# Optimization experiments

Hardware: AMD Instinct MI355X
Metric: run time of the kernel (lower is better)

Reference implementation:

```python
import jax, jax.numpy as jnp
import numpy as np

ALPHA = 0.2      # LeakyReLU negative slope
EPS = 1e-5       # LayerNorm eps (torch default)
NEG = -9e15      # mask value from the original module

N, IN_F, OUT_F = 8192, 256, 64


def setup_inputs() -> dict:
    key = jax.random.key(0)
    k1, k2, k3, k4, k5 = jax.random.split(key, 5)
    inp = {
        "input": jax.random.normal(k1, (N, IN_F), dtype=jnp.float32),
        "adj": jax.random.randint(k2, (N, N), 0, 2, dtype=jnp.int32),
        "W": jax.random.normal(k3, (IN_F, OUT_F), dtype=jnp.float32) * (1.414 * (6.0 / (IN_F + OUT_F)) ** 0.5),
        "a1": jax.random.normal(k4, (OUT_F,), dtype=jnp.float32) * 0.2,
        "a2": jax.random.normal(k5, (OUT_F,), dtype=jnp.float32) * 0.2,
        "gamma": jnp.ones((OUT_F,), dtype=jnp.float32),
        "beta": jnp.zeros((OUT_F,), dtype=jnp.float32),
    }
    return inp


def reference(input, adj, W, a1, a2, gamma, beta):
    h = input @ W                                    # [N, F]
    # a^T [Wh_i || Wh_j] = (Wh_i @ a1) + (Wh_j @ a2)  (exact decomposition)
    f = h @ a1                                       # [N]
    g = h @ a2                                       # [N]
    e = jax.nn.leaky_relu(f[:, None] + g[None, :], ALPHA)   # [N, N]
    e = jnp.where(adj > 0, e, jnp.float32(NEG))
    attention = jax.nn.softmax(e, axis=1)            # [N, N]  (dropout p=0 -> identity)
    h_prime = attention @ h                          # [N, F]
    # LayerNorm over feature dim
    mu = jnp.mean(h_prime, axis=-1, keepdims=True)
    var = jnp.mean((h_prime - mu) ** 2, axis=-1, keepdims=True)
    h_norm = (h_prime - mu) * jax.lax.rsqrt(var + EPS) * gamma + beta
    return jax.nn.elu(h_norm)                        # concat=True -> ELU
```

## Files before the change

kernel.cpp:

```cpp
#include <hip/hip_runtime.h>
#include <math.h>

#define N      8192
#define IN_F   256
#define OUT_F  64
#define ALPHA  0.2f
#define LN_EPS 1e-5f
#define KVB    256
#define NCH    (N / KVB)

typedef __attribute__((ext_vector_type(8))) short bf16x8;
typedef __attribute__((ext_vector_type(4))) short s16x4;
typedef __attribute__((ext_vector_type(4))) float f32x4;
typedef __attribute__((ext_vector_type(4))) int   i32x4;

__device__ __forceinline__ float wave_sum(float v) {
#pragma unroll
    for (int off = 32; off >= 1; off >>= 1) v += __shfl_xor(v, off, 64);
    return v;
}

__device__ __forceinline__ short f2bf(float x) {
    union { float f; unsigned u; } v; v.f = x;
    unsigned r = v.u + 0x7FFF + ((v.u >> 16) & 1);
    return (short)(r >> 16);
}
__device__ __forceinline__ float bf2f(short b) {
    union { unsigned u; float f; } v; v.u = ((unsigned)(unsigned short)b) << 16;
    return v.f;
}

__global__ __launch_bounds__(256) void gat_phaseA(
    const float* __restrict__ input, const float* __restrict__ W,
    const float* __restrict__ a1, const float* __restrict__ a2,
    unsigned short* __restrict__ hB, float* __restrict__ fv, float* __restrict__ gv)
{
    const int lane = threadIdx.x & 63;
    const int wid  = threadIdx.x >> 6;
    const int blockRow0 = blockIdx.x * 32;
    const int i0 = blockRow0 + wid * 8;

    float hacc[8];
#pragma unroll
    for (int r = 0; r < 8; r++) hacc[r] = 0.f;

    for (int k = 0; k < IN_F; k += 4) {
        const float w0 = W[(k + 0) * OUT_F + lane];
        const float w1 = W[(k + 1) * OUT_F + lane];
        const float w2 = W[(k + 2) * OUT_F + lane];
        const float w3 = W[(k + 3) * OUT_F + lane];
#pragma unroll
        for (int r = 0; r < 8; r++) {
            const float4 iv = *(const float4*)&input[(size_t)(i0 + r) * IN_F + k];
            hacc[r] = fmaf(iv.x, w0, hacc[r]);
            hacc[r] = fmaf(iv.y, w1, hacc[r]);
            hacc[r] = fmaf(iv.z, w2, hacc[r]);
            hacc[r] = fmaf(iv.w, w3, hacc[r]);
        }
    }

    const float a1v = a1[lane];
    const float a2v = a2[lane];

    __shared__ float hsm[32][65];
#pragma unroll
    for (int r = 0; r < 8; r++) {
        hsm[wid * 8 + r][lane] = hacc[r];
        const float fr = wave_sum(hacc[r] * a1v);
        const float gr = wave_sum(hacc[r] * a2v);
        if (lane == 0) { fv[i0 + r] = fr; gv[i0 + r] = gr; }
    }
    __syncthreads();

    const int f  = threadIdx.x >> 2;
    const int cp = threadIdx.x & 3;
    union { unsigned short s[8]; int4 v; } pk;
#pragma unroll
    for (int c = 0; c < 8; c++) pk.s[c] = (unsigned short)f2bf(hsm[cp * 8 + c][f]);
    *(int4*)&hB[(size_t)((blockRow0 >> 3) + cp) * 512 + f * 8] = pk.v;
}

__global__ __launch_bounds__(256) void gat_attn(
    const int* __restrict__ adj, const unsigned short* __restrict__ hB,
    const float* __restrict__ fv, const float* __restrict__ gv,
    const float* __restrict__ gamma, const float* __restrict__ beta,
    float* __restrict__ out)
{
    __shared__ short wls[16][264];
    __shared__ float lnbuf[16][68];
    __shared__ float denbuf[16];

    const int tid  = threadIdx.x;
    const int lane = tid & 63;
    const int wid  = tid >> 6;
    const int n16  = lane & 15;
    const int g4   = lane >> 4;
    const int rowBase = blockIdx.x * 16;
    const int rbase   = rowBase + wid * 4;

    float frow[4];
#pragma unroll
    for (int rr = 0; rr < 4; ++rr) frow[rr] = fv[rbase + rr];

    f32x4 acc = {0.f, 0.f, 0.f, 0.f};
    float dp[4] = {0.f, 0.f, 0.f, 0.f};

    i32x4  adjA[4], adjB[4];
    float4 gA, gB;

#define PREFETCH(JP, ADJ, G) do {                                              \
    _Pragma("unroll")                                                          \
    for (int rr = 0; rr < 4; ++rr)                                             \
        ADJ[rr] = __builtin_nontemporal_load(                                  \
            (const i32x4*)(adj + (size_t)(rbase + rr) * N + (JP) + lane * 4)); \
    G = *(const float4*)(gv + (JP) + lane * 4);                                \
} while (0)

#define STEP(C, ADJ, G, NADJ, NG) do {                                         \
        \
    bf16x8 breg[8];                                                            \
    {                                                                          \
        const unsigned short* hb = hB + (size_t)((C) * 32 + g4) * 512          \
                                   + wid * 128 + n16 * 8;                      \
        _Pragma("unroll")                                                      \
        for (int ks = 0; ks < 8; ++ks)                                         \
            breg[ks] = *(const bf16x8*)(hb + (size_t)ks * 2048);               \
    }                                                                          \
    const int pc = ((C) + 1 < NCH) ? (C) + 1 : (C);                            \
    PREFETCH((size_t)pc * KVB, NADJ, NG);                                      \
    __syncthreads();                    \
    _Pragma("unroll")                                                          \
    for (int rr = 0; rr < 4; ++rr) {                                           \
        s16x4 pk;                                                              \
        _Pragma("unroll")                                                      \
        for (int e = 0; e < 4; ++e) {                                          \
            float t = frow[rr] + ((const float*)&G)[e];                        \
            t = fmaxf(t, ALPHA * t);                           \
            const float w = (((const int*)&ADJ[rr])[e] > 0) ? __expf(t) : 0.f; \
            const short wb = f2bf(w);                                          \
            dp[rr] += bf2f(wb);                                                \
            pk[e] = wb;                                                        \
        }                                                                      \
        *(s16x4*)&wls[wid * 4 + rr][lane * 4] = pk;                            \
    }                                                                          \
    __syncthreads();                                          \
    _Pragma("unroll")                                                          \
    for (int ks = 0; ks < 8; ++ks) {                                           \
        bf16x8 a = *(const bf16x8*)&wls[n16][ks * 32 + g4 * 8];                \
        acc = __builtin_amdgcn_mfma_f32_16x16x32_bf16(a, breg[ks], acc, 0, 0, 0); \
    }                                                                          \
} while (0)

    PREFETCH(0, adjA, gA);
    for (int c = 0; c < NCH; c += 2) {
        STEP(c,     adjA, gA, adjB, gB);
        STEP(c + 1, adjB, gB, adjA, gA);
    }
#undef STEP
#undef PREFETCH

#pragma unroll
    for (int rr = 0; rr < 4; ++rr) {
        const float dr = wave_sum(dp[rr]);
        if (lane == 0) denbuf[wid * 4 + rr] = dr;
    }

#pragma unroll
    for (int r = 0; r < 4; ++r) lnbuf[g4 * 4 + r][wid * 16 + n16] = acc[r];
    __syncthreads();

    const int r = tid >> 4;
    const int q = tid & 15;
    const float den = denbuf[r];
    float4 v = *(const float4*)&lnbuf[r][q * 4];
    const float inv = 1.0f / den;
    v.x *= inv; v.y *= inv; v.z *= inv; v.w *= inv;

    float sm = v.x + v.y + v.z + v.w;
#pragma unroll
    for (int o = 1; o < 16; o <<= 1) sm += __shfl_xor(sm, o, 64);
    const float mu = sm * (1.0f / 64.0f);

    const float dx = v.x - mu, dy = v.y - mu, dz = v.z - mu, dw = v.w - mu;
    float ss = dx * dx + dy * dy + dz * dz + dw * dw;
#pragma unroll
    for (int o = 1; o < 16; o <<= 1) ss += __shfl_xor(ss, o, 64);
    const float rs = rsqrtf(ss * (1.0f / 64.0f) + LN_EPS);

    const float4 gm = *(const float4*)&gamma[q * 4];
    const float4 bt = *(const float4*)&beta[q * 4];
    float y0 = dx * rs * gm.x + bt.x;
    float y1 = dy * rs * gm.y + bt.y;
    float y2 = dz * rs * gm.z + bt.z;
    float y3 = dw * rs * gm.w + bt.w;
    y0 = (y0 > 0.f) ? y0 : expm1f(y0);
    y1 = (y1 > 0.f) ? y1 : expm1f(y1);
    y2 = (y2 > 0.f) ? y2 : expm1f(y2);
    y3 = (y3 > 0.f) ? y3 : expm1f(y3);
    *(float4*)&out[(size_t)(rowBase + r) * OUT_F + q * 4] = make_float4(y0, y1, y2, y3);
}

extern "C" void kernel_launch(void* const* d_in, const int* in_sizes, int n_in,
                              void* d_out, int out_size, void* d_ws, size_t ws_size,
                              hipStream_t stream)
{
    const float* input = (const float*)d_in[0];
    const int*   adj   = (const int*)d_in[1];
    const float* W     = (const float*)d_in[2];
    const float* a1    = (const float*)d_in[3];
    const float* a2    = (const float*)d_in[4];
    const float* gamma = (const float*)d_in[5];
    const float* beta  = (const float*)d_in[6];
    float* out = (float*)d_out;

    unsigned short* hB = (unsigned short*)d_ws;
    float* fv = (float*)(hB + (size_t)OUT_F * N);
    float* gv = fv + N;

    gat_phaseA<<<N / 32, 256, 0, stream>>>(input, W, a1, a2, hB, fv, gv);
    gat_attn<<<N / 16, 256, 0, stream>>>(adj, hB, fv, gv, gamma, beta, out);
}
```

Baseline: 89.22 us.

## Split attention key range across two wave groups per block and merge partials

```diff
diff --git a/kernel.cpp b/kernel.cpp
--- a/kernel.cpp
+++ b/kernel.cpp
@@ -7,7 +7,7 @@
 #define ALPHA  0.2f
 #define LN_EPS 1e-5f
 #define KVB    256
-#define NCH    (N / KVB)
+#define NCHH   16
 
 typedef __attribute__((ext_vector_type(8))) short bf16x8;
 typedef __attribute__((ext_vector_type(4))) short s16x4;
@@ -80,23 +80,25 @@
     *(int4*)&hB[(size_t)((blockRow0 >> 3) + cp) * 512 + f * 8] = pk.v;
 }
 
-__global__ __launch_bounds__(256) void gat_attn(
+__global__ __launch_bounds__(512, 4) void gat_attn(
     const int* __restrict__ adj, const unsigned short* __restrict__ hB,
     const float* __restrict__ fv, const float* __restrict__ gv,
     const float* __restrict__ gamma, const float* __restrict__ beta,
     float* __restrict__ out)
 {
-    __shared__ short wls[16][264];
+    __shared__ short wls[2][16][264];
     __shared__ float lnbuf[16][68];
-    __shared__ float denbuf[16];
+    __shared__ float denbuf[2][16];
 
     const int tid  = threadIdx.x;
     const int lane = tid & 63;
     const int wid  = tid >> 6;
+    const int H    = wid >> 2;
+    const int w4   = wid & 3;
     const int n16  = lane & 15;
     const int g4   = lane >> 4;
     const int rowBase = blockIdx.x * 16;
-    const int rbase   = rowBase + wid * 4;
+    const int rbase   = rowBase + w4 * 4;
 
     float frow[4];
 #pragma unroll
@@ -108,26 +110,28 @@
     i32x4  adjA[4], adjB[4];
     float4 gA, gB;
 
-#define PREFETCH(JP, ADJ, G) do {                                              \
+#define PREFETCH(GC, ADJ, G) do {                                              \
+    const size_t jp = (size_t)(GC) * KVB;                                      \
     _Pragma("unroll")                                                          \
     for (int rr = 0; rr < 4; ++rr)                                             \
         ADJ[rr] = __builtin_nontemporal_load(                                  \
-            (const i32x4*)(adj + (size_t)(rbase + rr) * N + (JP) + lane * 4)); \
-    G = *(const float4*)(gv + (JP) + lane * 4);                                \
+            (const i32x4*)(adj + (size_t)(rbase + rr) * N + jp + lane * 4));   \
+    G = *(const float4*)(gv + jp + lane * 4);                                  \
 } while (0)
 
 #define STEP(C, ADJ, G, NADJ, NG) do {                                         \
-        \
+    const int gc = H * NCHH + (C);                                             \
+            \
     bf16x8 breg[8];                                                            \
     {                                                                          \
-        const unsigned short* hb = hB + (size_t)((C) * 32 + g4) * 512          \
-                                   + wid * 128 + n16 * 8;                      \
+        const unsigned short* hb = hB + (size_t)(gc * 32 + g4) * 512           \
+                                   + w4 * 128 + n16 * 8;                       \
         _Pragma("unroll")                                                      \
         for (int ks = 0; ks < 8; ++ks)                                         \
             breg[ks] = *(const bf16x8*)(hb + (size_t)ks * 2048);               \
     }                                                                          \
-    const int pc = ((C) + 1 < NCH) ? (C) + 1 : (C);                            \
-    PREFETCH((size_t)pc * KVB, NADJ, NG);                                      \
+    const int pcc = ((C) + 1 < NCHH) ? (C) + 1 : (C);                          \
+    PREFETCH(H * NCHH + pcc, NADJ, NG);                                        \
     __syncthreads();                    \
     _Pragma("unroll")                                                          \
     for (int rr = 0; rr < 4; ++rr) {                                           \
@@ -141,18 +145,18 @@
             dp[rr] += bf2f(wb);                                                \
             pk[e] = wb;                                                        \
         }                                                                      \
-        *(s16x4*)&wls[wid * 4 + rr][lane * 4] = pk;                            \
+        *(s16x4*)&wls[H][w4 * 4 + rr][lane * 4] = pk;                          \
     }                                                                          \
     __syncthreads();                                          \
     _Pragma("unroll")                                                          \
     for (int ks = 0; ks < 8; ++ks) {                                           \
-        bf16x8 a = *(const bf16x8*)&wls[n16][ks * 32 + g4 * 8];                \
+        bf16x8 a = *(const bf16x8*)&wls[H][n16][ks * 32 + g4 * 8];             \
         acc = __builtin_amdgcn_mfma_f32_16x16x32_bf16(a, breg[ks], acc, 0, 0, 0); \
     }                                                                          \
 } while (0)
 
-    PREFETCH(0, adjA, gA);
-    for (int c = 0; c < NCH; c += 2) {
+    PREFETCH(H * NCHH, adjA, gA);
+    for (int c = 0; c < NCHH; c += 2) {
         STEP(c,     adjA, gA, adjB, gB);
         STEP(c + 1, adjB, gB, adjA, gA);
     }
@@ -162,42 +166,51 @@
 #pragma unroll
     for (int rr = 0; rr < 4; ++rr) {
         const float dr = wave_sum(dp[rr]);
-        if (lane == 0) denbuf[wid * 4 + rr] = dr;
-    }
-
-#pragma unroll
-    for (int r = 0; r < 4; ++r) lnbuf[g4 * 4 + r][wid * 16 + n16] = acc[r];
+        if (lane == 0) denbuf[H][w4 * 4 + rr] = dr;
+    }
+
+    if (H == 0) {
+#pragma unroll
+        for (int r = 0; r < 4; ++r) lnbuf[g4 * 4 + r][w4 * 16 + n16] = acc[r];
+    }
     __syncthreads();
-
-    const int r = tid >> 4;
-    const int q = tid & 15;
-    const float den = denbuf[r];
-    float4 v = *(const float4*)&lnbuf[r][q * 4];
-    const float inv = 1.0f / den;
-    v.x *= inv; v.y *= inv; v.z *= inv; v.w *= inv;
-
-    float sm = v.x + v.y + v.z + v.w;
-#pragma unroll
-    for (int o = 1; o < 16; o <<= 1) sm += __shfl_xor(sm, o, 64);
-    const float mu = sm * (1.0f / 64.0f);
-
-    const float dx = v.x - mu, dy = v.y - mu, dz = v.z - mu, dw = v.w - mu;
-    float ss = dx * dx + dy * dy + dz * dz + dw * dw;
-#pragma unroll
-    for (int o = 1; o < 16; o <<= 1) ss += __shfl_xor(ss, o, 64);
-    const float rs = rsqrtf(ss * (1.0f / 64.0f) + LN_EPS);
-
-    const float4 gm = *(const float4*)&gamma[q * 4];
-    const float4 bt = *(const float4*)&beta[q * 4];
-    float y0 = dx * rs * gm.x + bt.x;
-    float y1 = dy * rs * gm.y + bt.y;
-    float y2 = dz * rs * gm.z + bt.z;
-    float y3 = dw * rs * gm.w + bt.w;
-    y0 = (y0 > 0.f) ? y0 : expm1f(y0);
-    y1 = (y1 > 0.f) ? y1 : expm1f(y1);
-    y2 = (y2 > 0.f) ? y2 : expm1f(y2);
-    y3 = (y3 > 0.f) ? y3 : expm1f(y3);
-    *(float4*)&out[(size_t)(rowBase + r) * OUT_F + q * 4] = make_float4(y0, y1, y2, y3);
+    if (H == 1) {
+#pragma unroll
+        for (int r = 0; r < 4; ++r) lnbuf[g4 * 4 + r][w4 * 16 + n16] += acc[r];
+    }
+    __syncthreads();
+
+    if (tid < 256) {
+        const int r = tid >> 4;
+        const int q = tid & 15;
+        const float den = denbuf[0][r] + denbuf[1][r];
+        float4 v = *(const float4*)&lnbuf[r][q * 4];
+        const float inv = 1.0f / den;
+        v.x *= inv; v.y *= inv; v.z *= inv; v.w *= inv;
+
+        float sm = v.x + v.y + v.z + v.w;
+#pragma unroll
+        for (int o = 1; o < 16; o <<= 1) sm += __shfl_xor(sm, o, 64);
+        const float mu = sm * (1.0f / 64.0f);
+
+        const float dx = v.x - mu, dy = v.y - mu, dz = v.z - mu, dw = v.w - mu;
+        float ss = dx * dx + dy * dy + dz * dz + dw * dw;
+#pragma unroll
+        for (int o = 1; o < 16; o <<= 1) ss += __shfl_xor(ss, o, 64);
+        const float rs = rsqrtf(ss * (1.0f / 64.0f) + LN_EPS);
+
+        const float4 gm = *(const float4*)&gamma[q * 4];
+        const float4 bt = *(const float4*)&beta[q * 4];
+        float y0 = dx * rs * gm.x + bt.x;
+        float y1 = dy * rs * gm.y + bt.y;
+        float y2 = dz * rs * gm.z + bt.z;
+        float y3 = dw * rs * gm.w + bt.w;
+        y0 = (y0 > 0.f) ? y0 : expm1f(y0);
+        y1 = (y1 > 0.f) ? y1 : expm1f(y1);
+        y2 = (y2 > 0.f) ? y2 : expm1f(y2);
+        y3 = (y3 > 0.f) ? y3 : expm1f(y3);
+        *(float4*)&out[(size_t)(rowBase + r) * OUT_F + q * 4] = make_float4(y0, y1, y2, y3);
+    }
 }
 
 extern "C" void kernel_launch(void* const* d_in, const int* in_sizes, int n_in,
@@ -218,5 +231,5 @@
     float* gv = fv + N;
 
     gat_phaseA<<<N / 32, 256, 0, stream>>>(input, W, a1, a2, hB, fv, gv);
-    gat_attn<<<N / 16, 256, 0, stream>>>(adj, hB, fv, gv, gamma, beta, out);
-}
+    gat_attn<<<N / 16, 512, 0, stream>>>(adj, hB, fv, gv, gamma, beta, out);
+}
```

After: 107.5 us. 20.5% more time.

## Split attention columns across waves and reduce partial accumulators in LDS

Applied to the files above, without the earlier changes.

```diff
diff --git a/kernel.cpp b/kernel.cpp
--- a/kernel.cpp
+++ b/kernel.cpp
@@ -6,8 +6,9 @@
 #define OUT_F  64
 #define ALPHA  0.2f
 #define LN_EPS 1e-5f
-#define KVB    256
-#define NCH    (N / KVB)
+#define CQ     2048
+#define CSTEP  256
+#define NSTEP  (CQ / CSTEP)
 
 typedef __attribute__((ext_vector_type(8))) short bf16x8;
 typedef __attribute__((ext_vector_type(4))) short s16x4;
@@ -86,9 +87,9 @@
     const float* __restrict__ gamma, const float* __restrict__ beta,
     float* __restrict__ out)
 {
-    __shared__ short wls[16][264];
-    __shared__ float lnbuf[16][68];
-    __shared__ float denbuf[16];
+    __shared__ short wtile[4][16][264];
+    __shared__ float lnacc[4][16][68];
+    __shared__ float dpls[4][16];
 
     const int tid  = threadIdx.x;
     const int lane = tid & 63;
@@ -96,92 +97,89 @@
     const int n16  = lane & 15;
     const int g4   = lane >> 4;
     const int rowBase = blockIdx.x * 16;
-    const int rbase   = rowBase + wid * 4;
-
-    float frow[4];
-#pragma unroll
-    for (int rr = 0; rr < 4; ++rr) frow[rr] = fv[rbase + rr];
-
-    f32x4 acc = {0.f, 0.f, 0.f, 0.f};
-    float dp[4] = {0.f, 0.f, 0.f, 0.f};
-
-    i32x4  adjA[4], adjB[4];
-    float4 gA, gB;
-
-#define PREFETCH(JP, ADJ, G) do {                                              \
-    _Pragma("unroll")                                                          \
-    for (int rr = 0; rr < 4; ++rr)                                             \
-        ADJ[rr] = __builtin_nontemporal_load(                                  \
-            (const i32x4*)(adj + (size_t)(rbase + rr) * N + (JP) + lane * 4)); \
-    G = *(const float4*)(gv + (JP) + lane * 4);                                \
-} while (0)
-
-#define STEP(C, ADJ, G, NADJ, NG) do {                                         \
-        \
-    bf16x8 breg[8];                                                            \
-    {                                                                          \
-        const unsigned short* hb = hB + (size_t)((C) * 32 + g4) * 512          \
-                                   + wid * 128 + n16 * 8;                      \
-        _Pragma("unroll")                                                      \
-        for (int ks = 0; ks < 8; ++ks)                                         \
-            breg[ks] = *(const bf16x8*)(hb + (size_t)ks * 2048);               \
-    }                                                                          \
-    const int pc = ((C) + 1 < NCH) ? (C) + 1 : (C);                            \
-    PREFETCH((size_t)pc * KVB, NADJ, NG);                                      \
-    __syncthreads();                    \
-    _Pragma("unroll")                                                          \
-    for (int rr = 0; rr < 4; ++rr) {                                           \
-        s16x4 pk;                                                              \
-        _Pragma("unroll")                                                      \
-        for (int e = 0; e < 4; ++e) {                                          \
-            float t = frow[rr] + ((const float*)&G)[e];                        \
-            t = fmaxf(t, ALPHA * t);                           \
-            const float w = (((const int*)&ADJ[rr])[e] > 0) ? __expf(t) : 0.f; \
-            const short wb = f2bf(w);                                          \
-            dp[rr] += bf2f(wb);                                                \
-            pk[e] = wb;                                                        \
-        }                                                                      \
-        *(s16x4*)&wls[wid * 4 + rr][lane * 4] = pk;                            \
-    }                                                                          \
-    __syncthreads();                                          \
-    _Pragma("unroll")                                                          \
-    for (int ks = 0; ks < 8; ++ks) {                                           \
-        bf16x8 a = *(const bf16x8*)&wls[n16][ks * 32 + g4 * 8];                \
-        acc = __builtin_amdgcn_mfma_f32_16x16x32_bf16(a, breg[ks], acc, 0, 0, 0); \
-    }                                                                          \
-} while (0)
-
-    PREFETCH(0, adjA, gA);
-    for (int c = 0; c < NCH; c += 2) {
-        STEP(c,     adjA, gA, adjB, gB);
-        STEP(c + 1, adjB, gB, adjA, gA);
-    }
-#undef STEP
-#undef PREFETCH
-
-#pragma unroll
-    for (int rr = 0; rr < 4; ++rr) {
-        const float dr = wave_sum(dp[rr]);
-        if (lane == 0) denbuf[wid * 4 + rr] = dr;
-    }
-
-#pragma unroll
-    for (int r = 0; r < 4; ++r) lnbuf[g4 * 4 + r][wid * 16 + n16] = acc[r];
+    const int cbase   = wid * CQ;
+
+    float frow[16];
+#pragma unroll
+    for (int q = 0; q < 4; ++q) {
+        const float4 fq = *(const float4*)&fv[rowBase + q * 4];
+        frow[q * 4 + 0] = fq.x; frow[q * 4 + 1] = fq.y;
+        frow[q * 4 + 2] = fq.z; frow[q * 4 + 3] = fq.w;
+    }
+
+    f32x4 acc[4];
+#pragma unroll
+    for (int fb = 0; fb < 4; ++fb) acc[fb] = (f32x4){0.f, 0.f, 0.f, 0.f};
+    float dp[16];
+#pragma unroll
+    for (int r = 0; r < 16; ++r) dp[r] = 0.f;
+
+    for (int st = 0; st < NSTEP; ++st) {
+        const int c0 = cbase + st * CSTEP;
+        const float4 g4v = *(const float4*)&gv[c0 + lane * 4];
+
+#pragma unroll
+        for (int r = 0; r < 16; ++r) {
+            const i32x4 av = *(const i32x4*)(adj + (size_t)(rowBase + r) * N + c0 + lane * 4);
+            s16x4 pk;
+#pragma unroll
+            for (int e = 0; e < 4; ++e) {
+                float t = frow[r] + ((const float*)&g4v)[e];
+                t = fmaxf(t, ALPHA * t);
+                const float w = (av[e] > 0) ? __expf(t) : 0.0f;
+                const short wb = f2bf(w);
+                dp[r] += bf2f(wb);
+                pk[e] = wb;
+            }
+            *(s16x4*)&wtile[wid][r][lane * 4] = pk;
+        }
+
+#pragma unroll
+        for (int ks = 0; ks < 8; ++ks) {
+            const bf16x8 a = *(const bf16x8*)&wtile[wid][n16][ks * 32 + g4 * 8];
+            const unsigned short* hb =
+                hB + ((size_t)(c0 + ks * 32 + g4 * 8) >> 3) * 512 + n16 * 8;
+#pragma unroll
+            for (int fb = 0; fb < 4; ++fb) {
+                const bf16x8 b = *(const bf16x8*)(hb + fb * 128);
+                acc[fb] = __builtin_amdgcn_mfma_f32_16x16x32_bf16(a, b, acc[fb], 0, 0, 0);
+            }
+        }
+    }
+
+#pragma unroll
+    for (int r = 0; r < 16; ++r) {
+        const float dr = wave_sum(dp[r]);
+        if (lane == 0) dpls[wid][r] = dr;
+    }
+
+#pragma unroll
+    for (int fb = 0; fb < 4; ++fb)
+#pragma unroll
+        for (int i = 0; i < 4; ++i)
+            lnacc[wid][g4 * 4 + i][fb * 16 + n16] = acc[fb][i];
+
     __syncthreads();
 
     const int r = tid >> 4;
     const int q = tid & 15;
-    const float den = denbuf[r];
-    float4 v = *(const float4*)&lnbuf[r][q * 4];
+    const float den = dpls[0][r] + dpls[1][r] + dpls[2][r] + dpls[3][r];
+    const float4 v0 = *(const float4*)&lnacc[0][r][q * 4];
+    const float4 v1 = *(const float4*)&lnacc[1][r][q * 4];
+    const float4 v2 = *(const float4*)&lnacc[2][r][q * 4];
+    const float4 v3 = *(const float4*)&lnacc[3][r][q * 4];
     const float inv = 1.0f / den;
-    v.x *= inv; v.y *= inv; v.z *= inv; v.w *= inv;
-
-    float sm = v.x + v.y + v.z + v.w;
+    float vx = (v0.x + v1.x + v2.x + v3.x) * inv;
+    float vy = (v0.y + v1.y + v2.y + v3.y) * inv;
+    float vz = (v0.z + v1.z + v2.z + v3.z) * inv;
+    float vw = (v0.w + v1.w + v2.w + v3.w) * inv;
+
+    float sm = vx + vy + vz + vw;
 #pragma unroll
     for (int o = 1; o < 16; o <<= 1) sm += __shfl_xor(sm, o, 64);
     const float mu = sm * (1.0f / 64.0f);
 
-    const float dx = v.x - mu, dy = v.y - mu, dz = v.z - mu, dw = v.w - mu;
+    const float dx = vx - mu, dy = vy - mu, dz = vz - mu, dw = vw - mu;
     float ss = dx * dx + dy * dy + dz * dz + dw * dw;
 #pragma unroll
     for (int o = 1; o < 16; o <<= 1) ss += __shfl_xor(ss, o, 64);
@@ -214,7 +212,7 @@
     float* out = (float*)d_out;
 
     unsigned short* hB = (unsigned short*)d_ws;
-    float* fv = (float*)(hB + (size_t)OUT_F * N);
+    float* fv = (float*)((char*)d_ws + 1048576);
     float* gv = fv + N;
 
     gat_phaseA<<<N / 32, 256, 0, stream>>>(input, W, a1, a2, hB, fv, gv);
```

Result: slower. 157.4 us (+76.5%).
